# Optimization experiments

Measured on AMD Instinct MI355X. Metric: run time of the kernel, lower is better.

The kernel has to match this reference:

```python
import jax, jax.numpy as jnp
import numpy as np

N = 50000      # atoms
E = 800000     # edges (flat neighbor list)
ELEM = 64      # elem_fea_len
NBR = 64       # nbr_fea_len
EPS = 1e-5


def _bn(x, gamma, beta):
    # BatchNorm1d in training mode: biased batch stats over dim 0
    mean = jnp.mean(x, axis=0)
    var = jnp.mean(jnp.square(x - mean), axis=0)
    return (x - mean) * jax.lax.rsqrt(var + EPS) * gamma + beta


def setup_inputs() -> dict:
    key = jax.random.key(0)
    ks = jax.random.split(key, 8)
    atom_in_fea = jax.random.normal(ks[0], (N, ELEM), dtype=jnp.float32)
    nbr_fea = jax.random.normal(ks[1], (E, NBR), dtype=jnp.float32)
    self_fea_idx = jnp.sort(jax.random.randint(ks[2], (E,), 0, N))
    nbr_fea_idx = jax.random.randint(ks[3], (E,), 0, N)
    d_in = 2 * ELEM + NBR
    d_out = 2 * ELEM
    W = jax.random.normal(ks[4], (d_in, d_out), dtype=jnp.float32) / np.sqrt(d_in)
    b = jax.random.normal(ks[5], (d_out,), dtype=jnp.float32) * 0.01
    bn1_gamma = jnp.ones((d_out,), jnp.float32)
    bn1_beta = jnp.zeros((d_out,), jnp.float32)
    bn2_gamma = jnp.ones((ELEM,), jnp.float32)
    bn2_beta = jnp.zeros((ELEM,), jnp.float32)
    return {
        "atom_in_fea": atom_in_fea, "nbr_fea": nbr_fea,
        "self_fea_idx": self_fea_idx, "nbr_fea_idx": nbr_fea_idx,
        "W": W, "b": b,
        "bn1_gamma": bn1_gamma, "bn1_beta": bn1_beta,
        "bn2_gamma": bn2_gamma, "bn2_beta": bn2_beta,
    }


def reference(atom_in_fea, nbr_fea, self_fea_idx, nbr_fea_idx,
              W, b, bn1_gamma, bn1_beta, bn2_gamma, bn2_beta):
    n_atoms = atom_in_fea.shape[0]
    # gather endpoint features: (E, ELEM) each
    atom_self = atom_in_fea[self_fea_idx]
    atom_nbr = atom_in_fea[nbr_fea_idx]
    total = jnp.concatenate([atom_self, atom_nbr, nbr_fea], axis=1)  # (E, 2*ELEM+NBR)
    total = total @ W + b                                            # (E, 2*ELEM)
    total = _bn(total, bn1_gamma, bn1_beta)
    filter_fea, core_fea = jnp.split(total, 2, axis=1)
    nbr_msg = jax.nn.sigmoid(filter_fea) * jax.nn.softplus(core_fea)  # (E, ELEM)
    nbr_sumed = jax.ops.segment_sum(nbr_msg, self_fea_idx, num_segments=n_atoms)
    nbr_sumed = _bn(nbr_sumed, bn2_gamma, bn2_beta)
    return jax.nn.softplus(atom_in_fea + nbr_sumed)
```

## Files before the change

### kernel.cpp

```cpp
#include <hip/hip_runtime.h>

typedef unsigned short ushort_t;
typedef __attribute__((ext_vector_type(8))) short short8;
typedef __attribute__((ext_vector_type(4))) float f32x4;
typedef __attribute__((ext_vector_type(4))) float vf4;

constexpr int N_ATOMS = 50000;
constexpr int N_EDGES = 800000;
constexpr int ELEM    = 64;
constexpr int D_IN    = 192;
constexpr int D_OUT   = 128;
constexpr float EPS   = 1e-5f;

constexpr int TILE_M = 64;
constexpr int NREP   = 16;

constexpr size_t OFF_NS   = 0;
constexpr size_t OFF_ABF  = OFF_NS   + (size_t)N_ATOMS * ELEM * 4;
constexpr size_t OFF_NBF  = OFF_ABF  + (size_t)N_ATOMS * ELEM * 2;
constexpr size_t OFF_WT   = OFF_NBF  + (size_t)N_EDGES * ELEM * 2;
constexpr size_t OFF_BN1  = OFF_WT   + (size_t)D_OUT * D_IN * 2;
constexpr size_t OFF_BN2  = OFF_BN1  + NREP * 256 * 4;

__device__ __forceinline__ ushort_t f32_to_bf16(float f) {
    unsigned int u = __float_as_uint(f);
    u = (u + 0x7fffu + ((u >> 16) & 1u)) >> 16;
    return (ushort_t)u;
}
__device__ __forceinline__ float softplus_f(float x) {
    return fmaxf(x, 0.f) + __logf(1.f + __expf(-fabsf(x)));
}

__global__ void prep_init_kernel(const float* __restrict__ atom, const float* __restrict__ W,
                                 ushort_t* __restrict__ abf, ushort_t* __restrict__ Wt,
                                 float* __restrict__ ns,
                                 float* __restrict__ bn1r, float* __restrict__ bn2r) {
    int i = blockIdx.x * blockDim.x + threadIdx.x;
    if (i < N_ATOMS * ELEM) { abf[i] = f32_to_bf16(atom[i]); ns[i] = 0.f; }
    if (i < D_IN * D_OUT) {
        int k = i >> 7, n = i & 127;
        Wt[n * D_IN + k] = f32_to_bf16(W[i]);
    }
    if (i < NREP * 256) bn1r[i] = 0.f;
    if (i < NREP * 128) bn2r[i] = 0.f;
}

__device__ __forceinline__ void stage_atoms(ushort_t (*As)[200],
                                            const ushort_t* __restrict__ abf,
                                            const int* __restrict__ sidx,
                                            const int* __restrict__ nidx,
                                            int e0, int tid) {
    #pragma unroll
    for (int ch = 0; ch < 2; ++ch) {
        const int* __restrict__ idx = ch ? nidx : sidx;
        #pragma unroll
        for (int i = 0; i < 2; ++i) {
            int r = (tid >> 3) + 32 * i;
            int h = tid & 7;
            const uint4* src = (const uint4*)(abf + (size_t)idx[e0 + r] * 64);
            *(uint4*)&As[r][ch * 64 + h * 8] = src[h];
        }
    }
}

__global__ __launch_bounds__(256) void stats_kernel(
    const ushort_t* __restrict__ abf, const float* __restrict__ nbrf,
    const int* __restrict__ sidx, const int* __restrict__ nidx,
    const ushort_t* __restrict__ Wt, const float* __restrict__ bias,
    ushort_t* __restrict__ nbrf_bf, float* __restrict__ bn1r)
{
    __shared__ __align__(16) ushort_t As[64][200];
    const int tid = threadIdx.x;
    const int e0  = blockIdx.x * TILE_M;

    stage_atoms(As, abf, sidx, nidx, e0, tid);
    #pragma unroll
    for (int i = 0; i < 4; ++i) {
        int r  = (tid >> 4) + 16 * i;
        int c4 = tid & 15;
        vf4 v = __builtin_nontemporal_load((const vf4*)(nbrf + (size_t)(e0 + r) * 64 + c4 * 4));
        ushort4 pk;
        pk.x = f32_to_bf16(v.x); pk.y = f32_to_bf16(v.y);
        pk.z = f32_to_bf16(v.z); pk.w = f32_to_bf16(v.w);
        *(ushort4*)&As[r][128 + c4 * 4] = pk;
        *(ushort4*)&nbrf_bf[(size_t)(e0 + r) * 64 + c4 * 4] = pk;
    }

    const int wave = tid >> 6, lane = tid & 63;
    const int m16 = lane & 15, quad = lane >> 4;

    f32x4 acc[4][2];
    #pragma unroll
    for (int mt = 0; mt < 4; ++mt)
        #pragma unroll
        for (int nt = 0; nt < 2; ++nt) acc[mt][nt] = (f32x4){0.f, 0.f, 0.f, 0.f};

    const ushort_t* bp0 = Wt + (size_t)(wave * 32 + m16) * D_IN + quad * 8;
    const ushort_t* bp1 = bp0 + 16 * D_IN;

    __syncthreads();

    #pragma unroll
    for (int h = 0; h < 2; ++h) {
        short8 b0[3], b1[3];
        #pragma unroll
        for (int ks = 0; ks < 3; ++ks) {
            b0[ks] = *(const short8*)(bp0 + (h * 3 + ks) * 32);
            b1[ks] = *(const short8*)(bp1 + (h * 3 + ks) * 32);
        }
        #pragma unroll
        for (int ks = 0; ks < 3; ++ks) {
            int ko = (h * 3 + ks) * 32 + quad * 8;
            #pragma unroll
            for (int mt = 0; mt < 4; ++mt) {
                short8 a = *(const short8*)&As[mt * 16 + m16][ko];
                acc[mt][0] = __builtin_amdgcn_mfma_f32_16x16x32_bf16(a, b0[ks], acc[mt][0], 0, 0, 0);
                acc[mt][1] = __builtin_amdgcn_mfma_f32_16x16x32_bf16(a, b1[ks], acc[mt][1], 0, 0, 0);
            }
        }
    }

    float* rep = bn1r + (size_t)(blockIdx.x & (NREP - 1)) * 256;
    #pragma unroll
    for (int nt = 0; nt < 2; ++nt) {
        int c = wave * 32 + nt * 16 + m16;
        float b = bias[c];
        float s = 0.f, q = 0.f;
        #pragma unroll
        for (int mt = 0; mt < 4; ++mt)
            #pragma unroll
            for (int r = 0; r < 4; ++r) {
                float v = acc[mt][nt][r] + b;
                s += v; q += v * v;
            }
        s += __shfl_xor(s, 16); s += __shfl_xor(s, 32);
        q += __shfl_xor(q, 16); q += __shfl_xor(q, 32);
        if (quad == 0) {
            atomicAdd(&rep[c], s);
            atomicAdd(&rep[128 + c], q);
        }
    }
}

__global__ __launch_bounds__(256) void msg_kernel(
    const ushort_t* __restrict__ abf, const ushort_t* __restrict__ nbrf_bf,
    const int* __restrict__ sidx, const int* __restrict__ nidx,
    const ushort_t* __restrict__ Wt, const float* __restrict__ bias,
    const float* __restrict__ bn1r, const float* __restrict__ g1,
    const float* __restrict__ b1, float* __restrict__ ns)
{
    __shared__ __align__(16) char smem[25600];
    ushort_t (*As)[200] = (ushort_t(*)[200])smem;
    float    (*Ms)[68]  = (float(*)[68])smem;
    __shared__ int ss[64];
    __shared__ float scs[256];

    const int tid = threadIdx.x;
    const int e0  = blockIdx.x * TILE_M;

    if (tid < 128) {
        int c = tid;
        float s = 0.f, q = 0.f;
        #pragma unroll
        for (int r = 0; r < NREP; ++r) { s += bn1r[r * 256 + c]; q += bn1r[r * 256 + 128 + c]; }
        float mean = s * (1.f / N_EDGES);
        float var  = q * (1.f / N_EDGES) - mean * mean;
        float scale = g1[c] * rsqrtf(var + EPS);
        scs[c] = scale;
        scs[128 + c] = fmaf(bias[c] - mean, scale, b1[c]);
    }

    stage_atoms(As, abf, sidx, nidx, e0, tid);
    #pragma unroll
    for (int i = 0; i < 2; ++i) {
        int r = (tid >> 3) + 32 * i;
        int h = tid & 7;
        const uint4* src = (const uint4*)(nbrf_bf + (size_t)(e0 + r) * 64);
        *(uint4*)&As[r][128 + h * 8] = src[h];
    }
    if (tid < 64) ss[tid] = sidx[e0 + tid];

    const int wave = tid >> 6, lane = tid & 63;
    const int m16 = lane & 15, quad = lane >> 4;
    const int cf = wave * 16 + m16;
    const int cc = 64 + cf;

    f32x4 acc[4][2];
    #pragma unroll
    for (int mt = 0; mt < 4; ++mt)
        #pragma unroll
        for (int nt = 0; nt < 2; ++nt) acc[mt][nt] = (f32x4){0.f, 0.f, 0.f, 0.f};

    const ushort_t* bp0 = Wt + (size_t)cf * D_IN + quad * 8;
    const ushort_t* bp1 = Wt + (size_t)cc * D_IN + quad * 8;

    __syncthreads();

    #pragma unroll
    for (int h = 0; h < 2; ++h) {
        short8 b0[3], b1v[3];
        #pragma unroll
        for (int ks = 0; ks < 3; ++ks) {
            b0[ks]  = *(const short8*)(bp0 + (h * 3 + ks) * 32);
            b1v[ks] = *(const short8*)(bp1 + (h * 3 + ks) * 32);
        }
        #pragma unroll
        for (int ks = 0; ks < 3; ++ks) {
            int ko = (h * 3 + ks) * 32 + quad * 8;
            #pragma unroll
            for (int mt = 0; mt < 4; ++mt) {
                short8 a = *(const short8*)&As[mt * 16 + m16][ko];
                acc[mt][0] = __builtin_amdgcn_mfma_f32_16x16x32_bf16(a, b0[ks], acc[mt][0], 0, 0, 0);
                acc[mt][1] = __builtin_amdgcn_mfma_f32_16x16x32_bf16(a, b1v[ks], acc[mt][1], 0, 0, 0);
            }
        }
    }
    __syncthreads();

    {
        float scf = scs[cf], shf = scs[128 + cf];
        float scc = scs[cc], shc = scs[128 + cc];
        #pragma unroll
        for (int mt = 0; mt < 4; ++mt) {
            int row = mt * 16 + quad * 4;
            #pragma unroll
            for (int r = 0; r < 4; ++r) {
                float yf = fmaf(acc[mt][0][r], scf, shf);
                float yc = fmaf(acc[mt][1][r], scc, shc);
                Ms[row + r][cf] = softplus_f(yc) / (1.f + __expf(-yf));
            }
        }
    }
    __syncthreads();

    {
        int v = tid >> 6, c = tid & 63;
        int base = v * 16;
        int cur = ss[base];
        float a = 0.f;
        #pragma unroll
        for (int r = 0; r < 16; ++r) {
            int s = ss[base + r];
            if (s != cur) { atomicAdd(&ns[(size_t)cur * 64 + c], a); cur = s; a = 0.f; }
            a += Ms[base + r][c];
        }
        atomicAdd(&ns[(size_t)cur * 64 + c], a);
    }
}

__global__ __launch_bounds__(256) void bn2_stats_kernel(
    const float* __restrict__ ns, float* __restrict__ bn2r)
{
    int c = threadIdx.x & 63;
    float s = 0.f, q = 0.f;
    for (int a = blockIdx.x * 4 + (threadIdx.x >> 6); a < N_ATOMS; a += 4096) {
        float v = ns[a * ELEM + c];
        s += v; q += v * v;
    }
    float* rep = bn2r + (size_t)(blockIdx.x & (NREP - 1)) * 128;
    atomicAdd(&rep[c], s);
    atomicAdd(&rep[64 + c], q);
}

__global__ __launch_bounds__(256) void final_kernel(
    const float* __restrict__ atom, const float* __restrict__ ns,
    const float* __restrict__ bn2r, const float* __restrict__ g2,
    const float* __restrict__ b2, float* __restrict__ out)
{
    __shared__ float sc2s[128];
    int t = threadIdx.x;
    if (t < 64) {
        float s = 0.f, q = 0.f;
        #pragma unroll
        for (int r = 0; r < NREP; ++r) { s += bn2r[r * 128 + t]; q += bn2r[r * 128 + 64 + t]; }
        float mean = s * (1.f / N_ATOMS);
        float var  = q * (1.f / N_ATOMS) - mean * mean;
        float scale = g2[t] * rsqrtf(var + EPS);
        sc2s[t] = scale;
        sc2s[64 + t] = b2[t] - mean * scale;
    }
    __syncthreads();
    int i = blockIdx.x * 256 + t;
    if (i < N_ATOMS * ELEM) {
        int c = t & 63;
        float x = atom[i] + fmaf(ns[i], sc2s[c], sc2s[64 + c]);
        out[i] = softplus_f(x);
    }
}

extern "C" void kernel_launch(void* const* d_in, const int* in_sizes, int n_in,
                              void* d_out, int out_size, void* d_ws, size_t ws_size,
                              hipStream_t stream) {
    const float* atom = (const float*)d_in[0];
    const float* nbrf = (const float*)d_in[1];
    const int*   sidx = (const int*)d_in[2];
    const int*   nidx = (const int*)d_in[3];
    const float* W    = (const float*)d_in[4];
    const float* bias = (const float*)d_in[5];
    const float* g1   = (const float*)d_in[6];
    const float* b1   = (const float*)d_in[7];
    const float* g2   = (const float*)d_in[8];
    const float* b2   = (const float*)d_in[9];
    float* out = (float*)d_out;
    char*  ws  = (char*)d_ws;

    float*    ns    = (float*)(ws + OFF_NS);
    ushort_t* abf   = (ushort_t*)(ws + OFF_ABF);
    ushort_t* nbf   = (ushort_t*)(ws + OFF_NBF);
    ushort_t* Wt    = (ushort_t*)(ws + OFF_WT);
    float*    bn1r  = (float*)(ws + OFF_BN1);
    float*    bn2r  = (float*)(ws + OFF_BN2);

    hipLaunchKernelGGL(prep_init_kernel, dim3((N_ATOMS * ELEM + 255) / 256), dim3(256), 0, stream,
                       atom, W, abf, Wt, ns, bn1r, bn2r);
    hipLaunchKernelGGL(stats_kernel, dim3(N_EDGES / TILE_M), dim3(256), 0, stream,
                       abf, nbrf, sidx, nidx, Wt, bias, nbf, bn1r);
    hipLaunchKernelGGL(msg_kernel, dim3(N_EDGES / TILE_M), dim3(256), 0, stream,
                       abf, nbf, sidx, nidx, Wt, bias, bn1r, g1, b1, ns);
    hipLaunchKernelGGL(bn2_stats_kernel, dim3(1024), dim3(256), 0, stream, ns, bn2r);
    hipLaunchKernelGGL(final_kernel, dim3((N_ATOMS * ELEM + 255) / 256), dim3(256), 0, stream,
                       atom, ns, bn2r, g2, b2, out);
}
```

Baseline: 498.4 us.

## Store bf16 GEMM output in stats pass instead of recomputing in message pass

```diff
diff --git a/kernel.cpp b/kernel.cpp
--- a/kernel.cpp
+++ b/kernel.cpp
@@ -12,20 +12,25 @@
 constexpr int D_OUT   = 128;
 constexpr float EPS   = 1e-5f;
 
-constexpr int TILE_M = 64;
-constexpr int NREP   = 16;
+constexpr int TILE_M  = 64;
+constexpr int N_TILES = N_EDGES / TILE_M;
+constexpr int NREP    = 16;
 
 constexpr size_t OFF_NS   = 0;
 constexpr size_t OFF_ABF  = OFF_NS   + (size_t)N_ATOMS * ELEM * 4;
-constexpr size_t OFF_NBF  = OFF_ABF  + (size_t)N_ATOMS * ELEM * 2;
-constexpr size_t OFF_WT   = OFF_NBF  + (size_t)N_EDGES * ELEM * 2;
+constexpr size_t OFF_WT   = OFF_ABF  + (size_t)N_ATOMS * ELEM * 2;
 constexpr size_t OFF_BN1  = OFF_WT   + (size_t)D_OUT * D_IN * 2;
-constexpr size_t OFF_BN2  = OFF_BN1  + NREP * 256 * 4;
+constexpr size_t OFF_SC1  = OFF_BN1  + NREP * 256 * 4;
+constexpr size_t OFF_BN2  = OFF_SC1  + 256 * 4;
+constexpr size_t OFF_T2   = OFF_BN2  + NREP * 128 * 4;
 
 __device__ __forceinline__ ushort_t f32_to_bf16(float f) {
     unsigned int u = __float_as_uint(f);
     u = (u + 0x7fffu + ((u >> 16) & 1u)) >> 16;
     return (ushort_t)u;
+}
+__device__ __forceinline__ float bf16_to_f32(ushort_t h) {
+    return __uint_as_float(((unsigned int)h) << 16);
 }
 __device__ __forceinline__ float softplus_f(float x) {
     return fmaxf(x, 0.f) + __logf(1.f + __expf(-fabsf(x)));
@@ -66,8 +71,8 @@
 __global__ __launch_bounds__(256) void stats_kernel(
     const ushort_t* __restrict__ abf, const float* __restrict__ nbrf,
     const int* __restrict__ sidx, const int* __restrict__ nidx,
-    const ushort_t* __restrict__ Wt, const float* __restrict__ bias,
-    ushort_t* __restrict__ nbrf_bf, float* __restrict__ bn1r)
+    const ushort_t* __restrict__ Wt,
+    ushort_t* __restrict__ T2, float* __restrict__ bn1r)
 {
     __shared__ __align__(16) ushort_t As[64][200];
     const int tid = threadIdx.x;
@@ -83,7 +88,6 @@
         pk.x = f32_to_bf16(v.x); pk.y = f32_to_bf16(v.y);
         pk.z = f32_to_bf16(v.z); pk.w = f32_to_bf16(v.w);
         *(ushort4*)&As[r][128 + c4 * 4] = pk;
-        *(ushort4*)&nbrf_bf[(size_t)(e0 + r) * 64 + c4 * 4] = pk;
     }
 
     const int wave = tid >> 6, lane = tid & 63;
@@ -120,17 +124,29 @@
         }
     }
 
-    float* rep = bn1r + (size_t)(blockIdx.x & (NREP - 1)) * 256;
+    ushort_t* tp = T2 + (size_t)blockIdx.x * 128 * 64;
     #pragma unroll
     for (int nt = 0; nt < 2; ++nt) {
         int c = wave * 32 + nt * 16 + m16;
-        float b = bias[c];
+        #pragma unroll
+        for (int mt = 0; mt < 4; ++mt) {
+            uint2 u;
+            u.x = (unsigned)f32_to_bf16(acc[mt][nt][0]) | ((unsigned)f32_to_bf16(acc[mt][nt][1]) << 16);
+            u.y = (unsigned)f32_to_bf16(acc[mt][nt][2]) | ((unsigned)f32_to_bf16(acc[mt][nt][3]) << 16);
+            *(uint2*)&tp[c * 64 + mt * 16 + quad * 4] = u;
+        }
+    }
+
+    float* rep = bn1r + (size_t)(blockIdx.x & (NREP - 1)) * 256;
+    #pragma unroll
+    for (int nt = 0; nt < 2; ++nt) {
+        int c = wave * 32 + nt * 16 + m16;
         float s = 0.f, q = 0.f;
         #pragma unroll
         for (int mt = 0; mt < 4; ++mt)
             #pragma unroll
             for (int r = 0; r < 4; ++r) {
-                float v = acc[mt][nt][r] + b;
+                float v = acc[mt][nt][r];
                 s += v; q += v * v;
             }
         s += __shfl_xor(s, 16); s += __shfl_xor(s, 32);
@@ -142,110 +158,67 @@
     }
 }
 
+__global__ void bn1_finalize(const float* __restrict__ bn1r,
+                             const float* __restrict__ g1, const float* __restrict__ b1,
+                             float* __restrict__ sc) {
+    int c = threadIdx.x;
+    float s = 0.f, q = 0.f;
+    #pragma unroll
+    for (int r = 0; r < NREP; ++r) { s += bn1r[r * 256 + c]; q += bn1r[r * 256 + 128 + c]; }
+    float mean = s * (1.f / N_EDGES);
+    float var  = q * (1.f / N_EDGES) - mean * mean;
+    float scale = g1[c] * rsqrtf(var + EPS);
+    sc[c] = scale;
+    sc[128 + c] = b1[c] - mean * scale;
+}
+
 __global__ __launch_bounds__(256) void msg_kernel(
-    const ushort_t* __restrict__ abf, const ushort_t* __restrict__ nbrf_bf,
-    const int* __restrict__ sidx, const int* __restrict__ nidx,
-    const ushort_t* __restrict__ Wt, const float* __restrict__ bias,
-    const float* __restrict__ bn1r, const float* __restrict__ g1,
-    const float* __restrict__ b1, float* __restrict__ ns)
-{
-    __shared__ __align__(16) char smem[25600];
-    ushort_t (*As)[200] = (ushort_t(*)[200])smem;
-    float    (*Ms)[68]  = (float(*)[68])smem;
-    __shared__ int ss[64];
-    __shared__ float scs[256];
-
-    const int tid = threadIdx.x;
-    const int e0  = blockIdx.x * TILE_M;
-
-    if (tid < 128) {
-        int c = tid;
-        float s = 0.f, q = 0.f;
-        #pragma unroll
-        for (int r = 0; r < NREP; ++r) { s += bn1r[r * 256 + c]; q += bn1r[r * 256 + 128 + c]; }
-        float mean = s * (1.f / N_EDGES);
-        float var  = q * (1.f / N_EDGES) - mean * mean;
-        float scale = g1[c] * rsqrtf(var + EPS);
-        scs[c] = scale;
-        scs[128 + c] = fmaf(bias[c] - mean, scale, b1[c]);
-    }
-
-    stage_atoms(As, abf, sidx, nidx, e0, tid);
-    #pragma unroll
-    for (int i = 0; i < 2; ++i) {
-        int r = (tid >> 3) + 32 * i;
-        int h = tid & 7;
-        const uint4* src = (const uint4*)(nbrf_bf + (size_t)(e0 + r) * 64);
-        *(uint4*)&As[r][128 + h * 8] = src[h];
-    }
-    if (tid < 64) ss[tid] = sidx[e0 + tid];
-
+    const ushort_t* __restrict__ T2, const int* __restrict__ sidx,
+    const float* __restrict__ sc, float* __restrict__ ns)
+{
+    __shared__ int ss[256];
+    const int tid  = threadIdx.x;
     const int wave = tid >> 6, lane = tid & 63;
-    const int m16 = lane & 15, quad = lane >> 4;
-    const int cf = wave * 16 + m16;
-    const int cc = 64 + cf;
-
-    f32x4 acc[4][2];
-    #pragma unroll
-    for (int mt = 0; mt < 4; ++mt)
-        #pragma unroll
-        for (int nt = 0; nt < 2; ++nt) acc[mt][nt] = (f32x4){0.f, 0.f, 0.f, 0.f};
-
-    const ushort_t* bp0 = Wt + (size_t)cf * D_IN + quad * 8;
-    const ushort_t* bp1 = Wt + (size_t)cc * D_IN + quad * 8;
+    const int tile = blockIdx.x * 4 + wave;
+    const int e0   = tile * TILE_M;
+
+    ss[tid] = sidx[blockIdx.x * 256 + tid];
+
+    const ushort_t* fp = T2 + (size_t)tile * 128 * 64 + lane * 64;
+    const ushort_t* cp = fp + 64 * 64;
+    float scf = sc[lane],      shf = sc[128 + lane];
+    float scc = sc[64 + lane], shc = sc[192 + lane];
 
     __syncthreads();
 
-    #pragma unroll
-    for (int h = 0; h < 2; ++h) {
-        short8 b0[3], b1v[3];
-        #pragma unroll
-        for (int ks = 0; ks < 3; ++ks) {
-            b0[ks]  = *(const short8*)(bp0 + (h * 3 + ks) * 32);
-            b1v[ks] = *(const short8*)(bp1 + (h * 3 + ks) * 32);
-        }
-        #pragma unroll
-        for (int ks = 0; ks < 3; ++ks) {
-            int ko = (h * 3 + ks) * 32 + quad * 8;
-            #pragma unroll
-            for (int mt = 0; mt < 4; ++mt) {
-                short8 a = *(const short8*)&As[mt * 16 + m16][ko];
-                acc[mt][0] = __builtin_amdgcn_mfma_f32_16x16x32_bf16(a, b0[ks], acc[mt][0], 0, 0, 0);
-                acc[mt][1] = __builtin_amdgcn_mfma_f32_16x16x32_bf16(a, b1v[ks], acc[mt][1], 0, 0, 0);
+    const int* sst = ss + wave * 64;
+    int cur = sst[0];
+    float acc = 0.f;
+    #pragma unroll
+    for (int ch = 0; ch < 8; ++ch) {
+        uint4 fv = *(const uint4*)(fp + ch * 8);
+        uint4 cv = *(const uint4*)(cp + ch * 8);
+        const unsigned* fw = (const unsigned*)&fv;
+        const unsigned* cw = (const unsigned*)&cv;
+        #pragma unroll
+        for (int j = 0; j < 8; ++j) {
+            int r = ch * 8 + j;
+            int s = sst[r];
+            if (s != cur) {
+                atomicAdd(&ns[(size_t)cur * 64 + lane], acc);
+                cur = s; acc = 0.f;
             }
-        }
-    }
-    __syncthreads();
-
-    {
-        float scf = scs[cf], shf = scs[128 + cf];
-        float scc = scs[cc], shc = scs[128 + cc];
-        #pragma unroll
-        for (int mt = 0; mt < 4; ++mt) {
-            int row = mt * 16 + quad * 4;
-            #pragma unroll
-            for (int r = 0; r < 4; ++r) {
-                float yf = fmaf(acc[mt][0][r], scf, shf);
-                float yc = fmaf(acc[mt][1][r], scc, shc);
-                Ms[row + r][cf] = softplus_f(yc) / (1.f + __expf(-yf));
-            }
-        }
-    }
-    __syncthreads();
-
-    {
-        int v = tid >> 6, c = tid & 63;
-        int base = v * 16;
-        int cur = ss[base];
-        float a = 0.f;
-        #pragma unroll
-        for (int r = 0; r < 16; ++r) {
-            int s = ss[base + r];
-            if (s != cur) { atomicAdd(&ns[(size_t)cur * 64 + c], a); cur = s; a = 0.f; }
-            a += Ms[base + r][c];
-        }
-        atomicAdd(&ns[(size_t)cur * 64 + c], a);
-    }
+            unsigned wf = fw[j >> 1], wc = cw[j >> 1];
+            float tf = (j & 1) ? __uint_as_float(wf & 0xffff0000u)
+                               : __uint_as_float(wf << 16);
+            float tc = (j & 1) ? __uint_as_float(wc & 0xffff0000u)
+                               : __uint_as_float(wc << 16);
+            float yf = fmaf(tf, scf, shf);
+            float yc = fmaf(tc, scc, shc);
+            acc += softplus_f(yc) / (1.f + __expf(-yf));
+        }
+    }
+    atomicAdd(&ns[(size_t)cur * 64 + lane], acc);
 }
 
 __global__ __launch_bounds__(256) void bn2_stats_kernel(
@@ -296,7 +269,6 @@
     const int*   sidx = (const int*)d_in[2];
     const int*   nidx = (const int*)d_in[3];
     const float* W    = (const float*)d_in[4];
-    const float* bias = (const float*)d_in[5];
     const float* g1   = (const float*)d_in[6];
     const float* b1   = (const float*)d_in[7];
     const float* g2   = (const float*)d_in[8];
@@ -306,17 +278,19 @@
 
     float*    ns    = (float*)(ws + OFF_NS);
     ushort_t* abf   = (ushort_t*)(ws + OFF_ABF);
-    ushort_t* nbf   = (ushort_t*)(ws + OFF_NBF);
     ushort_t* Wt    = (ushort_t*)(ws + OFF_WT);
     float*    bn1r  = (float*)(ws + OFF_BN1);
+    float*    sc1   = (float*)(ws + OFF_SC1);
     float*    bn2r  = (float*)(ws + OFF_BN2);
+    ushort_t* T2    = (ushort_t*)(ws + OFF_T2);
 
     hipLaunchKernelGGL(prep_init_kernel, dim3((N_ATOMS * ELEM + 255) / 256), dim3(256), 0, stream,
                        atom, W, abf, Wt, ns, bn1r, bn2r);
-    hipLaunchKernelGGL(stats_kernel, dim3(N_EDGES / TILE_M), dim3(256), 0, stream,
-                       abf, nbrf, sidx, nidx, Wt, bias, nbf, bn1r);
-    hipLaunchKernelGGL(msg_kernel, dim3(N_EDGES / TILE_M), dim3(256), 0, stream,
-                       abf, nbf, sidx, nidx, Wt, bias, bn1r, g1, b1, ns);
+    hipLaunchKernelGGL(stats_kernel, dim3(N_TILES), dim3(256), 0, stream,
+                       abf, nbrf, sidx, nidx, Wt, T2, bn1r);
+    hipLaunchKernelGGL(bn1_finalize, dim3(1), dim3(128), 0, stream, bn1r, g1, b1, sc1);
+    hipLaunchKernelGGL(msg_kernel, dim3(N_TILES / 4), dim3(256), 0, stream,
+                       T2, sidx, sc1, ns);
     hipLaunchKernelGGL(bn2_stats_kernel, dim3(1024), dim3(256), 0, stream, ns, bn2r);
     hipLaunchKernelGGL(final_kernel, dim3((N_ATOMS * ELEM + 255) / 256), dim3(256), 0, stream,
                        atom, ns, bn2r, g2, b2, out);
```

Result: slower. 643.9 us (+29.2%).
